# Kernel tuning notes

Measured on AMD Instinct MI355X. Metric: run time of the kernel, lower is better.

The kernel has to match this reference:

```python
import jax, jax.numpy as jnp
import numpy as np

D = 64      # d_model
H = 8       # n_head
HS = D // H # head_size = 8
EPS = 1e-5


def _layernorm(x, g, b):
    m = jnp.mean(x, axis=-1, keepdims=True)
    v = jnp.var(x, axis=-1, keepdims=True)
    return (x - m) * jax.lax.rsqrt(v + EPS) * g + b


def _attn(x, Wq, bq, Wk, bk, Wv, bv, Wp, bp, causal):
    # x: [B,T,D]; Wq/Wk/Wv: [H,D,HS]; bq/bk/bv: [H,HS]; Wp: [D,D]; bp: [D]
    B, T, _ = x.shape
    q = jnp.einsum('btd,hds->bhts', x, Wq) + bq[:, None, :]
    k = jnp.einsum('btd,hds->bhts', x, Wk) + bk[:, None, :]
    v = jnp.einsum('btd,hds->bhts', x, Wv) + bv[:, None, :]
    wei = jnp.einsum('bhts,bhus->bhtu', q, k) * (HS ** -0.5)
    if causal:
        mask = jnp.tril(jnp.ones((T, T), dtype=bool))
        wei = jnp.where(mask, wei, -jnp.inf)
    w = jax.nn.softmax(wei, axis=-1)
    out = jnp.einsum('bhtu,bhus->bhts', w, v)        # [B,H,T,HS]
    out = jnp.swapaxes(out, 1, 2).reshape(B, T, D)   # concat heads
    return out @ Wp + bp


def _ffn(x, W1, b1, W2, b2):
    return jax.nn.gelu(x @ W1 + b1, approximate=False) @ W2 + b2


def setup_inputs() -> dict:
    key = jax.random.key(0)
    ks = jax.random.split(key, 32)
    s = 0.02
    d = {'x': jax.random.normal(ks[0], (32768, 16, D), dtype=jnp.float32)}
    # unmasked attention params
    d['uWq'] = s * jax.random.normal(ks[1], (H, D, HS)); d['ubq'] = jnp.zeros((H, HS))
    d['uWk'] = s * jax.random.normal(ks[2], (H, D, HS)); d['ubk'] = jnp.zeros((H, HS))
    d['uWv'] = s * jax.random.normal(ks[3], (H, D, HS)); d['ubv'] = jnp.zeros((H, HS))
    d['uWp'] = s * jax.random.normal(ks[4], (D, D));     d['ubp'] = jnp.zeros((D,))
    # masked attention params
    d['mWq'] = s * jax.random.normal(ks[5], (H, D, HS)); d['mbq'] = jnp.zeros((H, HS))
    d['mWk'] = s * jax.random.normal(ks[6], (H, D, HS)); d['mbk'] = jnp.zeros((H, HS))
    d['mWv'] = s * jax.random.normal(ks[7], (H, D, HS)); d['mbv'] = jnp.zeros((H, HS))
    d['mWp'] = s * jax.random.normal(ks[8], (D, D));     d['mbp'] = jnp.zeros((D,))
    # feed-forward (shared across both FFN calls, as in the torch Block)
    d['fW1'] = s * jax.random.normal(ks[9], (D, 4 * D)); d['fb1'] = jnp.zeros((4 * D,))
    d['fW2'] = s * jax.random.normal(ks[10], (4 * D, D)); d['fb2'] = jnp.zeros((D,))
    # layernorms (norm1 and norm2 each reused twice, as in the torch Block)
    d['g1'] = jnp.ones((D,)); d['be1'] = jnp.zeros((D,))
    d['g2'] = jnp.ones((D,)); d['be2'] = jnp.zeros((D,))
    return d


def reference(x, uWq, ubq, uWk, ubk, uWv, ubv, uWp, ubp,
              mWq, mbq, mWk, mbk, mWv, mbv, mWp, mbp,
              fW1, fb1, fW2, fb2, g1, be1, g2, be2):
    x2 = x + _attn(_layernorm(x, g1, be1), uWq, ubq, uWk, ubk, uWv, ubv, uWp, ubp, causal=False)
    x = x2 + _ffn(_layernorm(x2, g2, be2), fW1, fb1, fW2, fb2)
    x2 = x + _attn(_layernorm(x, g1, be1), mWq, mbq, mWk, mbk, mWv, mbv, mWp, mbp, causal=True)
    x = x2 + _ffn(_layernorm(x2, g2, be2), fW1, fb1, fW2, fb2)
    return x
```

## Files before the change

kernel.cpp:

```cpp
#include <hip/hip_runtime.h>
#include <math.h>

typedef short bf16x8 __attribute__((ext_vector_type(8)));
typedef float f32x4 __attribute__((ext_vector_type(4)));

union BF { unsigned u[4]; bf16x8 v; };

__device__ __forceinline__ unsigned pk2(float a, float b) {
  unsigned ua = __float_as_uint(a), ub = __float_as_uint(b);
  ua = (ua + 0x7FFFu + ((ua >> 16) & 1u)) >> 16;
  ub = (ub + 0x7FFFu + ((ub >> 16) & 1u)) >> 16;
  return (ua & 0xFFFFu) | (ub << 16);
}

#define OFF_F1 32768
#define OFF_F2 49152

__global__ __launch_bounds__(256) void prep_w(
    const float* __restrict__ uWq, const float* __restrict__ uWk,
    const float* __restrict__ uWv, const float* __restrict__ uWp,
    const float* __restrict__ mWq, const float* __restrict__ mWk,
    const float* __restrict__ mWv, const float* __restrict__ mWp,
    const float* __restrict__ fW1, const float* __restrict__ fW2,
    unsigned short* __restrict__ ws)
{
  int e = blockIdx.x * blockDim.x + threadIdx.x;
  if (e >= 8192) return;
  int lane = e & 63;
  int fb   = e >> 6;
  int g = lane >> 4, li = lane & 15;
  unsigned short outv[8];
#pragma unroll
  for (int j = 0; j < 8; ++j) {
    float val;
    if (fb < 64) {
      int a  = fb >> 3;
      int mf = fb & 7;
      int m = mf >> 1, f = mf & 1;
      int k = f*32 + 4*g + (j&3) + 16*(j>>2);
      int n = 16*m + li;
      const float* W =
        (a==0)?uWq:(a==1)?uWk:(a==2)?uWv:(a==3)?uWp:
        (a==4)?mWq:(a==5)?mWk:(a==6)?mWv:mWp;
      if ((a & 3) != 3) val = W[(n>>3)*512 + k*8 + (n&7)];
      else              val = W[k*64 + n];
    } else if (fb < 96) {
      int mf = fb - 64;
      int m = mf >> 1, f = mf & 1;
      int k = f*32 + 4*g + (j&3) + 16*(j>>2);
      int n = 16*m + li;
      val = fW1[k*256 + n];
    } else {
      int mf = fb - 96;
      int m = mf >> 3, f = mf & 7;
      int k = f*32 + 4*g + (j&3) + 16*(j>>2);
      int n = 16*m + li;
      val = fW2[k*64 + n];
    }
    unsigned u = __float_as_uint(val);
    u = (u + 0x7FFFu + ((u >> 16) & 1u)) >> 16;
    outv[j] = (unsigned short)u;
  }
#pragma unroll
  for (int j = 0; j < 8; ++j) ws[(long)e*8 + j] = outv[j];
}

#define LDSP 72

__global__ __launch_bounds__(64, 2) void tblock_kern(
    const float* __restrict__ x,
    const float* __restrict__ ubq, const float* __restrict__ ubk,
    const float* __restrict__ ubv, const float* __restrict__ ubp,
    const float* __restrict__ mbq, const float* __restrict__ mbk,
    const float* __restrict__ mbv, const float* __restrict__ mbp,
    const float* __restrict__ fb1, const float* __restrict__ fb2,
    const float* __restrict__ g1, const float* __restrict__ be1,
    const float* __restrict__ g2, const float* __restrict__ be2,
    const unsigned short* __restrict__ wf,
    float* __restrict__ outp)
{
  __shared__ float KS[2][16][LDSP];
  __shared__ float VS[2][16][LDSP];

  const int lane = threadIdx.x;
  const int t = lane & 15, g = lane >> 4;
  const long sbase = (long)blockIdx.x * 2048;

  f32x4 R[2][4];
#pragma unroll
  for (int s = 0; s < 2; ++s)
#pragma unroll
    for (int m = 0; m < 4; ++m)
      R[s][m] = *(const f32x4*)(x + sbase + s*1024 + t*64 + 16*m + 4*g);

  auto ldA = [&](int base_bf16, int fbidx) -> bf16x8 {
    return *(const bf16x8*)(wf + base_bf16 + fbidx*512 + lane*8);
  };

  auto lnorm = [&](int s, const float* gp, const float* bp, BF bx[2]) {
    float sum = 0.f, sq = 0.f;
#pragma unroll
    for (int m = 0; m < 4; ++m)
#pragma unroll
      for (int r = 0; r < 4; ++r) { float v = R[s][m][r]; sum += v; sq += v*v; }
    sum += __shfl_xor(sum, 16); sum += __shfl_xor(sum, 32);
    sq  += __shfl_xor(sq , 16); sq  += __shfl_xor(sq , 32);
    float mean = sum * 0.015625f;
    float var  = sq  * 0.015625f - mean*mean;
    float rs = __builtin_amdgcn_rsqf(var + 1e-5f);
    float xn[4][4];
#pragma unroll
    for (int m = 0; m < 4; ++m) {
      f32x4 gm = *(const f32x4*)(gp + 16*m + 4*g);
      f32x4 bm = *(const f32x4*)(bp + 16*m + 4*g);
#pragma unroll
      for (int r = 0; r < 4; ++r)
        xn[m][r] = (R[s][m][r] - mean) * rs * gm[r] + bm[r];
    }
#pragma unroll
    for (int f = 0; f < 2; ++f)
#pragma unroll
      for (int mm = 0; mm < 2; ++mm) {
        bx[f].u[2*mm+0] = pk2(xn[2*f+mm][0], xn[2*f+mm][1]);
        bx[f].u[2*mm+1] = pk2(xn[2*f+mm][2], xn[2*f+mm][3]);
      }
  };

  auto attn = [&](int wq, int wk, int wv, int wp,
                  const float* bq, const float* bk, const float* bv,
                  const float* bpj, bool causal) {
    BF bx[2][2];
    lnorm(0, g1, be1, bx[0]);
    lnorm(1, g1, be1, bx[1]);

    f32x4 Q[2][4];
#pragma unroll
    for (int m = 0; m < 4; ++m) {
      bf16x8 a0 = ldA(wq, m*2+0), a1 = ldA(wq, m*2+1);
      f32x4 b4 = *(const f32x4*)(bq + 16*m + 4*g);
#pragma unroll
      for (int s = 0; s < 2; ++s) {
        f32x4 acc = {0.f,0.f,0.f,0.f};
        acc = __builtin_amdgcn_mfma_f32_16x16x32_bf16(a0, bx[s][0].v, acc, 0,0,0);
        acc = __builtin_amdgcn_mfma_f32_16x16x32_bf16(a1, bx[s][1].v, acc, 0,0,0);
#pragma unroll
        for (int r = 0; r < 4; ++r) acc[r] += b4[r];
        Q[s][m] = acc;
      }
    }
#pragma unroll
    for (int m = 0; m < 4; ++m) {
      bf16x8 a0 = ldA(wk, m*2+0), a1 = ldA(wk, m*2+1);
      f32x4 b4 = *(const f32x4*)(bk + 16*m + 4*g);
#pragma unroll
      for (int s = 0; s < 2; ++s) {
        f32x4 acc = {0.f,0.f,0.f,0.f};
        acc = __builtin_amdgcn_mfma_f32_16x16x32_bf16(a0, bx[s][0].v, acc, 0,0,0);
        acc = __builtin_amdgcn_mfma_f32_16x16x32_bf16(a1, bx[s][1].v, acc, 0,0,0);
#pragma unroll
        for (int r = 0; r < 4; ++r) acc[r] += b4[r];
        *(f32x4*)&KS[s][t][16*m + 4*g] = acc;
      }
    }
#pragma unroll
    for (int m = 0; m < 4; ++m) {
      bf16x8 a0 = ldA(wv, m*2+0), a1 = ldA(wv, m*2+1);
      f32x4 b4 = *(const f32x4*)(bv + 16*m + 4*g);
#pragma unroll
      for (int s = 0; s < 2; ++s) {
        f32x4 acc = {0.f,0.f,0.f,0.f};
        acc = __builtin_amdgcn_mfma_f32_16x16x32_bf16(a0, bx[s][0].v, acc, 0,0,0);
        acc = __builtin_amdgcn_mfma_f32_16x16x32_bf16(a1, bx[s][1].v, acc, 0,0,0);
#pragma unroll
        for (int r = 0; r < 4; ++r) acc[r] += b4[r];
        *(f32x4*)&VS[s][t][16*m + 4*g] = acc;
      }
    }

#pragma unroll
    for (int s = 0; s < 2; ++s) {
      f32x4 O[4];
#pragma unroll
      for (int mp = 0; mp < 2; ++mp) {
        float e[2][16];
#pragma unroll
        for (int u = 0; u < 16; ++u) {
          f32x4 k0 = *(const f32x4*)&KS[s][u][32*mp + 4*g];
          f32x4 k1 = *(const f32x4*)&KS[s][u][32*mp + 16 + 4*g];
          f32x4 q0 = Q[s][2*mp+0], q1 = Q[s][2*mp+1];
          e[0][u] = q0[0]*k0[0] + q0[1]*k0[1] + q0[2]*k0[2] + q0[3]*k0[3];
          e[1][u] = q1[0]*k1[0] + q1[1]*k1[1] + q1[2]*k1[2] + q1[3]*k1[3];
        }
#pragma unroll
        for (int mm = 0; mm < 2; ++mm)
#pragma unroll
          for (int u = 0; u < 16; ++u)
            e[mm][u] += __shfl_xor(e[mm][u], 16);
        float rden[2];
#pragma unroll
        for (int mm = 0; mm < 2; ++mm) {
          float den = 0.f;
#pragma unroll
          for (int u = 0; u < 16; ++u) {
            float ex = (causal && (u > t)) ? 0.f
                     : exp2f(e[mm][u] * 0.51006977f);
            e[mm][u] = ex; den += ex;
          }
          rden[mm] = __builtin_amdgcn_rcpf(den);
        }
        f32x4 acc0 = {0.f,0.f,0.f,0.f}, acc1 = {0.f,0.f,0.f,0.f};
#pragma unroll
        for (int u = 0; u < 16; ++u) {
          f32x4 v0 = *(const f32x4*)&VS[s][u][32*mp + 4*g];
          f32x4 v1 = *(const f32x4*)&VS[s][u][32*mp + 16 + 4*g];
#pragma unroll
          for (int r = 0; r < 4; ++r) {
            acc0[r] += e[0][u] * v0[r];
            acc1[r] += e[1][u] * v1[r];
          }
        }
#pragma unroll
        for (int r = 0; r < 4; ++r) {
          O[2*mp+0][r] = acc0[r] * rden[0];
          O[2*mp+1][r] = acc1[r] * rden[1];
        }
      }
#pragma unroll
      for (int f = 0; f < 2; ++f)
#pragma unroll
        for (int mm = 0; mm < 2; ++mm) {
          bx[s][f].u[2*mm+0] = pk2(O[2*f+mm][0], O[2*f+mm][1]);
          bx[s][f].u[2*mm+1] = pk2(O[2*f+mm][2], O[2*f+mm][3]);
        }
    }
#pragma unroll
    for (int m = 0; m < 4; ++m) {
      bf16x8 a0 = ldA(wp, m*2+0), a1 = ldA(wp, m*2+1);
      f32x4 b4 = *(const f32x4*)(bpj + 16*m + 4*g);
#pragma unroll
      for (int s = 0; s < 2; ++s) {
        f32x4 acc = {0.f,0.f,0.f,0.f};
        acc = __builtin_amdgcn_mfma_f32_16x16x32_bf16(a0, bx[s][0].v, acc, 0,0,0);
        acc = __builtin_amdgcn_mfma_f32_16x16x32_bf16(a1, bx[s][1].v, acc, 0,0,0);
#pragma unroll
        for (int r = 0; r < 4; ++r) R[s][m][r] += acc[r] + b4[r];
      }
    }
  };

  auto ffn = [&]() {
    BF bx[2][2];
    lnorm(0, g2, be2, bx[0]);
    lnorm(1, g2, be2, bx[1]);
    f32x4 yacc[2][4];
#pragma unroll
    for (int s = 0; s < 2; ++s)
#pragma unroll
      for (int m = 0; m < 4; ++m) yacc[s][m] = f32x4{0.f,0.f,0.f,0.f};
#pragma unroll
    for (int qt = 0; qt < 4; ++qt) {
      f32x4 h[2][4];
#pragma unroll
      for (int mt = 0; mt < 4; ++mt) {
        int ht = qt*4 + mt;
        bf16x8 a0 = ldA(OFF_F1, ht*2+0), a1 = ldA(OFF_F1, ht*2+1);
        f32x4 b4 = *(const f32x4*)(fb1 + 16*ht + 4*g);
#pragma unroll
        for (int s = 0; s < 2; ++s) {
          f32x4 acc = {0.f,0.f,0.f,0.f};
          acc = __builtin_amdgcn_mfma_f32_16x16x32_bf16(a0, bx[s][0].v, acc, 0,0,0);
          acc = __builtin_amdgcn_mfma_f32_16x16x32_bf16(a1, bx[s][1].v, acc, 0,0,0);
#pragma unroll
          for (int r = 0; r < 4; ++r) {
            float vv = acc[r] + b4[r];
            h[s][mt][r] = 0.5f * vv * (1.f + erff(vv * 0.70710678f));
          }
        }
      }
      BF bh[2][2];
#pragma unroll
      for (int s = 0; s < 2; ++s)
#pragma unroll
        for (int q2 = 0; q2 < 2; ++q2) {
          bh[s][q2].u[0] = pk2(h[s][2*q2+0][0], h[s][2*q2+0][1]);
          bh[s][q2].u[1] = pk2(h[s][2*q2+0][2], h[s][2*q2+0][3]);
          bh[s][q2].u[2] = pk2(h[s][2*q2+1][0], h[s][2*q2+1][1]);
          bh[s][q2].u[3] = pk2(h[s][2*q2+1][2], h[s][2*q2+1][3]);
        }
#pragma unroll
      for (int m = 0; m < 4; ++m)
#pragma unroll
        for (int q2 = 0; q2 < 2; ++q2) {
          bf16x8 a = ldA(OFF_F2, m*8 + qt*2 + q2);
#pragma unroll
          for (int s = 0; s < 2; ++s)
            yacc[s][m] = __builtin_amdgcn_mfma_f32_16x16x32_bf16(a, bh[s][q2].v, yacc[s][m], 0,0,0);
        }
    }
#pragma unroll
    for (int m = 0; m < 4; ++m) {
      f32x4 b4 = *(const f32x4*)(fb2 + 16*m + 4*g);
#pragma unroll
      for (int s = 0; s < 2; ++s)
#pragma unroll
        for (int r = 0; r < 4; ++r) R[s][m][r] += yacc[s][m][r] + b4[r];
    }
  };

  attn(0*4096, 1*4096, 2*4096, 3*4096, ubq, ubk, ubv, ubp, false);
  ffn();
  attn(4*4096, 5*4096, 6*4096, 7*4096, mbq, mbk, mbv, mbp, true);
  ffn();

#pragma unroll
  for (int s = 0; s < 2; ++s)
#pragma unroll
    for (int m = 0; m < 4; ++m)
      *(f32x4*)(outp + sbase + s*1024 + t*64 + 16*m + 4*g) = R[s][m];
}

extern "C" void kernel_launch(void* const* d_in, const int* in_sizes, int n_in,
                              void* d_out, int out_size, void* d_ws, size_t ws_size,
                              hipStream_t stream) {
  const float* x   = (const float*)d_in[0];
  const float* uWq = (const float*)d_in[1];
  const float* ubq = (const float*)d_in[2];
  const float* uWk = (const float*)d_in[3];
  const float* ubk = (const float*)d_in[4];
  const float* uWv = (const float*)d_in[5];
  const float* ubv = (const float*)d_in[6];
  const float* uWp = (const float*)d_in[7];
  const float* ubp = (const float*)d_in[8];
  const float* mWq = (const float*)d_in[9];
  const float* mbq = (const float*)d_in[10];
  const float* mWk = (const float*)d_in[11];
  const float* mbk = (const float*)d_in[12];
  const float* mWv = (const float*)d_in[13];
  const float* mbv = (const float*)d_in[14];
  const float* mWp = (const float*)d_in[15];
  const float* mbp = (const float*)d_in[16];
  const float* fW1 = (const float*)d_in[17];
  const float* fb1 = (const float*)d_in[18];
  const float* fW2 = (const float*)d_in[19];
  const float* fb2 = (const float*)d_in[20];
  const float* g1  = (const float*)d_in[21];
  const float* be1 = (const float*)d_in[22];
  const float* g2  = (const float*)d_in[23];
  const float* be2 = (const float*)d_in[24];

  unsigned short* ws = (unsigned short*)d_ws;

  prep_w<<<32, 256, 0, stream>>>(uWq, uWk, uWv, uWp, mWq, mWk, mWv, mWp,
                                 fW1, fW2, ws);
  tblock_kern<<<16384, 64, 0, stream>>>(x,
      ubq, ubk, ubv, ubp, mbq, mbk, mbv, mbp,
      fb1, fb2, g1, be1, g2, be2,
      (const unsigned short*)ws, (float*)d_out);
}
```

Measured before the change: 1.466 ms.

## Use tanh GELU, bf16 K/V in LDS, fused online softmax, bias-in-accumulator MFMAs

Replaces the erf-based GELU with a tanh-form approximation built from exp2 and a reciprocal. K and V are now stored as packed bf16 in shared memory instead of fp32, halving LDS traffic and footprint. The softmax and value accumulation are merged into a single loop over keys, so the per-row score arrays are gone. Biases are used as the initial MFMA accumulator, and the FFN output accumulates directly into the residual registers, which drops the separate yacc array. The tanh-form GELU and bf16 K/V both add numerical error compared with the reference.

Result: no change. 1.491 ms (+1.7%).

```diff
diff --git a/kernel.cpp b/kernel.cpp
--- a/kernel.cpp
+++ b/kernel.cpp
@@ -1,16 +1,27 @@
 #include <hip/hip_runtime.h>
-#include <math.h>
 
 typedef short bf16x8 __attribute__((ext_vector_type(8)));
 typedef float f32x4 __attribute__((ext_vector_type(4)));
-
-union BF { unsigned u[4]; bf16x8 v; };
+typedef unsigned u32x4 __attribute__((ext_vector_type(4)));
+typedef unsigned u32x2 __attribute__((ext_vector_type(2)));
 
 __device__ __forceinline__ unsigned pk2(float a, float b) {
   unsigned ua = __float_as_uint(a), ub = __float_as_uint(b);
   ua = (ua + 0x7FFFu + ((ua >> 16) & 1u)) >> 16;
   ub = (ub + 0x7FFFu + ((ub >> 16) & 1u)) >> 16;
   return (ua & 0xFFFFu) | (ub << 16);
+}
+__device__ __forceinline__ bf16x8 mkfrag(unsigned a, unsigned b, unsigned c, unsigned d) {
+  u32x4 t = {a, b, c, d};
+  return __builtin_bit_cast(bf16x8, t);
+}
+__device__ __forceinline__ float blo(unsigned u) { return __uint_as_float(u << 16); }
+__device__ __forceinline__ float bhi(unsigned u) { return __uint_as_float(u & 0xFFFF0000u); }
+
+__device__ __forceinline__ float gelu_f(float v) {
+  float y = 0.7978845608f * v * (1.f + 0.044715f * v * v);
+  float e = exp2f(y * 2.8853900818f);
+  return v * (1.f - __builtin_amdgcn_rcpf(e + 1.f));
 }
 
 #define OFF_F1 32768
@@ -65,7 +76,7 @@
   for (int j = 0; j < 8; ++j) ws[(long)e*8 + j] = outv[j];
 }
 
-#define LDSP 72
+#define NU 36
 
 __global__ __launch_bounds__(64, 2) void tblock_kern(
     const float* __restrict__ x,
@@ -79,8 +90,8 @@
     const unsigned short* __restrict__ wf,
     float* __restrict__ outp)
 {
-  __shared__ float KS[2][16][LDSP];
-  __shared__ float VS[2][16][LDSP];
+  __shared__ unsigned KS[2][16][NU];
+  __shared__ unsigned VS[2][16][NU];
 
   const int lane = threadIdx.x;
   const int t = lane & 15, g = lane >> 4;
@@ -97,7 +108,8 @@
     return *(const bf16x8*)(wf + base_bf16 + fbidx*512 + lane*8);
   };
 
-  auto lnorm = [&](int s, const float* gp, const float* bp, BF bx[2]) {
+  auto lnorm = [&](int s, const float* gp, const float* bp,
+                   bf16x8& b0, bf16x8& b1) {
     float sum = 0.f, sq = 0.f;
 #pragma unroll
     for (int m = 0; m < 4; ++m)
@@ -117,21 +129,18 @@
       for (int r = 0; r < 4; ++r)
         xn[m][r] = (R[s][m][r] - mean) * rs * gm[r] + bm[r];
     }
-#pragma unroll
-    for (int f = 0; f < 2; ++f)
-#pragma unroll
-      for (int mm = 0; mm < 2; ++mm) {
-        bx[f].u[2*mm+0] = pk2(xn[2*f+mm][0], xn[2*f+mm][1]);
-        bx[f].u[2*mm+1] = pk2(xn[2*f+mm][2], xn[2*f+mm][3]);
-      }
+    b0 = mkfrag(pk2(xn[0][0], xn[0][1]), pk2(xn[0][2], xn[0][3]),
+                pk2(xn[1][0], xn[1][1]), pk2(xn[1][2], xn[1][3]));
+    b1 = mkfrag(pk2(xn[2][0], xn[2][1]), pk2(xn[2][2], xn[2][3]),
+                pk2(xn[3][0], xn[3][1]), pk2(xn[3][2], xn[3][3]));
   };
 
   auto attn = [&](int wq, int wk, int wv, int wp,
                   const float* bq, const float* bk, const float* bv,
                   const float* bpj, bool causal) {
-    BF bx[2][2];
-    lnorm(0, g1, be1, bx[0]);
-    lnorm(1, g1, be1, bx[1]);
+    bf16x8 bx[2][2];
+    lnorm(0, g1, be1, bx[0][0], bx[0][1]);
+    lnorm(1, g1, be1, bx[1][0], bx[1][1]);
 
     f32x4 Q[2][4];
 #pragma unroll
@@ -139,14 +148,9 @@
       bf16x8 a0 = ldA(wq, m*2+0), a1 = ldA(wq, m*2+1);
       f32x4 b4 = *(const f32x4*)(bq + 16*m + 4*g);
 #pragma unroll
-      for (int s = 0; s < 2; ++s) {
-        f32x4 acc = {0.f,0.f,0.f,0.f};
-        acc = __builtin_amdgcn_mfma_f32_16x16x32_bf16(a0, bx[s][0].v, acc, 0,0,0);
-        acc = __builtin_amdgcn_mfma_f32_16x16x32_bf16(a1, bx[s][1].v, acc, 0,0,0);
-#pragma unroll
-        for (int r = 0; r < 4; ++r) acc[r] += b4[r];
-        Q[s][m] = acc;
-      }
+      for (int s = 0; s < 2; ++s)
+        Q[s][m] = __builtin_amdgcn_mfma_f32_16x16x32_bf16(
+            a1, bx[s][1], __builtin_amdgcn_mfma_f32_16x16x32_bf16(a0, bx[s][0], b4, 0,0,0), 0,0,0);
     }
 #pragma unroll
     for (int m = 0; m < 4; ++m) {
@@ -154,12 +158,9 @@
       f32x4 b4 = *(const f32x4*)(bk + 16*m + 4*g);
 #pragma unroll
       for (int s = 0; s < 2; ++s) {
-        f32x4 acc = {0.f,0.f,0.f,0.f};
-        acc = __builtin_amdgcn_mfma_f32_16x16x32_bf16(a0, bx[s][0].v, acc, 0,0,0);
-        acc = __builtin_amdgcn_mfma_f32_16x16x32_bf16(a1, bx[s][1].v, acc, 0,0,0);
-#pragma unroll
-        for (int r = 0; r < 4; ++r) acc[r] += b4[r];
-        *(f32x4*)&KS[s][t][16*m + 4*g] = acc;
+        f32x4 acc = __builtin_amdgcn_mfma_f32_16x16x32_bf16(
+            a1, bx[s][1], __builtin_amdgcn_mfma_f32_16x16x32_bf16(a0, bx[s][0], b4, 0,0,0), 0,0,0);
+        *(u32x2*)&KS[s][t][8*m + 2*g] = u32x2{pk2(acc[0], acc[1]), pk2(acc[2], acc[3])};
       }
     }
 #pragma unroll
@@ -168,12 +169,9 @@
       f32x4 b4 = *(const f32x4*)(bv + 16*m + 4*g);
 #pragma unroll
       for (int s = 0; s < 2; ++s) {
-        f32x4 acc = {0.f,0.f,0.f,0.f};
-        acc = __builtin_amdgcn_mfma_f32_16x16x32_bf16(a0, bx[s][0].v, acc, 0,0,0);
-        acc = __builtin_amdgcn_mfma_f32_16x16x32_bf16(a1, bx[s][1].v, acc, 0,0,0);
-#pragma unroll
-        for (int r = 0; r < 4; ++r) acc[r] += b4[r];
-        *(f32x4*)&VS[s][t][16*m + 4*g] = acc;
+        f32x4 acc = __builtin_amdgcn_mfma_f32_16x16x32_bf16(
+            a1, bx[s][1], __builtin_amdgcn_mfma_f32_16x16x32_bf16(a0, bx[s][0], b4, 0,0,0), 0,0,0);
+        *(u32x2*)&VS[s][t][8*m + 2*g] = u32x2{pk2(acc[0], acc[1]), pk2(acc[2], acc[3])};
       }
     }
 
@@ -182,128 +180,93 @@
       f32x4 O[4];
 #pragma unroll
       for (int mp = 0; mp < 2; ++mp) {
-        float e[2][16];
+        f32x4 q0 = Q[s][2*mp+0], q1 = Q[s][2*mp+1];
+        f32x4 acc0 = {0.f,0.f,0.f,0.f}, acc1 = {0.f,0.f,0.f,0.f};
+        float den0 = 0.f, den1 = 0.f;
 #pragma unroll
         for (int u = 0; u < 16; ++u) {
-          f32x4 k0 = *(const f32x4*)&KS[s][u][32*mp + 4*g];
-          f32x4 k1 = *(const f32x4*)&KS[s][u][32*mp + 16 + 4*g];
-          f32x4 q0 = Q[s][2*mp+0], q1 = Q[s][2*mp+1];
-          e[0][u] = q0[0]*k0[0] + q0[1]*k0[1] + q0[2]*k0[2] + q0[3]*k0[3];
-          e[1][u] = q1[0]*k1[0] + q1[1]*k1[1] + q1[2]*k1[2] + q1[3]*k1[3];
+          u32x2 kp0 = *(const u32x2*)&KS[s][u][16*mp + 2*g];
+          u32x2 kp1 = *(const u32x2*)&KS[s][u][16*mp + 8 + 2*g];
+          float d0 = q0[0]*blo(kp0[0]) + q0[1]*bhi(kp0[0])
+                   + q0[2]*blo(kp0[1]) + q0[3]*bhi(kp0[1]);
+          float d1 = q1[0]*blo(kp1[0]) + q1[1]*bhi(kp1[0])
+                   + q1[2]*blo(kp1[1]) + q1[3]*bhi(kp1[1]);
+          d0 += __shfl_xor(d0, 16);
+          d1 += __shfl_xor(d1, 16);
+          float ex0 = (causal && (u > t)) ? 0.f : exp2f(d0 * 0.51006977f);
+          float ex1 = (causal && (u > t)) ? 0.f : exp2f(d1 * 0.51006977f);
+          den0 += ex0; den1 += ex1;
+          u32x2 vp0 = *(const u32x2*)&VS[s][u][16*mp + 2*g];
+          u32x2 vp1 = *(const u32x2*)&VS[s][u][16*mp + 8 + 2*g];
+          acc0[0] += ex0*blo(vp0[0]); acc0[1] += ex0*bhi(vp0[0]);
+          acc0[2] += ex0*blo(vp0[1]); acc0[3] += ex0*bhi(vp0[1]);
+          acc1[0] += ex1*blo(vp1[0]); acc1[1] += ex1*bhi(vp1[0]);
+          acc1[2] += ex1*blo(vp1[1]); acc1[3] += ex1*bhi(vp1[1]);
         }
-#pragma unroll
-        for (int mm = 0; mm < 2; ++mm)
-#pragma unroll
-          for (int u = 0; u < 16; ++u)
-            e[mm][u] += __shfl_xor(e[mm][u], 16);
-        float rden[2];
-#pragma unroll
-        for (int mm = 0; mm < 2; ++mm) {
-          float den = 0.f;
-#pragma unroll
-          for (int u = 0; u < 16; ++u) {
-            float ex = (causal && (u > t)) ? 0.f
-                     : exp2f(e[mm][u] * 0.51006977f);
-            e[mm][u] = ex; den += ex;
-          }
-          rden[mm] = __builtin_amdgcn_rcpf(den);
-        }
-        f32x4 acc0 = {0.f,0.f,0.f,0.f}, acc1 = {0.f,0.f,0.f,0.f};
-#pragma unroll
-        for (int u = 0; u < 16; ++u) {
-          f32x4 v0 = *(const f32x4*)&VS[s][u][32*mp + 4*g];
-          f32x4 v1 = *(const f32x4*)&VS[s][u][32*mp + 16 + 4*g];
-#pragma unroll
-          for (int r = 0; r < 4; ++r) {
-            acc0[r] += e[0][u] * v0[r];
-            acc1[r] += e[1][u] * v1[r];
+        float rd0 = __builtin_amdgcn_rcpf(den0), rd1 = __builtin_amdgcn_rcpf(den1);
+#pragma unroll
+        for (int r = 0; r < 4; ++r) { O[2*mp+0][r] = acc0[r]*rd0; O[2*mp+1][r] = acc1[r]*rd1; }
+      }
+      bx[s][0] = mkfrag(pk2(O[0][0], O[0][1]), pk2(O[0][2], O[0][3]),
+                        pk2(O[1][0], O[1][1]), pk2(O[1][2], O[1][3]));
+      bx[s][1] = mkfrag(pk2(O[2][0], O[2][1]), pk2(O[2][2], O[2][3]),
+                        pk2(O[3][0], O[3][1]), pk2(O[3][2], O[3][3]));
+    }
+#pragma unroll
+    for (int m = 0; m < 4; ++m) {
+      bf16x8 a0 = ldA(wp, m*2+0), a1 = ldA(wp, m*2+1);
+      f32x4 b4 = *(const f32x4*)(bpj + 16*m + 4*g);
+#pragma unroll
+      for (int s = 0; s < 2; ++s) {
+        R[s][m] = __builtin_amdgcn_mfma_f32_16x16x32_bf16(
+            a1, bx[s][1], __builtin_amdgcn_mfma_f32_16x16x32_bf16(a0, bx[s][0], R[s][m], 0,0,0), 0,0,0);
+#pragma unroll
+        for (int r = 0; r < 4; ++r) R[s][m][r] += b4[r];
+      }
+    }
+  };
+
+  auto ffn = [&]() {
+    bf16x8 bx[2][2];
+    lnorm(0, g2, be2, bx[0][0], bx[0][1]);
+    lnorm(1, g2, be2, bx[1][0], bx[1][1]);
+#pragma unroll
+    for (int qt = 0; qt < 4; ++qt) {
+#pragma unroll
+      for (int q2 = 0; q2 < 2; ++q2) {
+        f32x4 h[2][2];
+#pragma unroll
+        for (int mt2 = 0; mt2 < 2; ++mt2) {
+          int ht = qt*4 + 2*q2 + mt2;
+          bf16x8 a0 = ldA(OFF_F1, ht*2+0), a1 = ldA(OFF_F1, ht*2+1);
+          f32x4 b4 = *(const f32x4*)(fb1 + 16*ht + 4*g);
+#pragma unroll
+          for (int s = 0; s < 2; ++s) {
+            f32x4 acc = __builtin_amdgcn_mfma_f32_16x16x32_bf16(
+                a1, bx[s][1], __builtin_amdgcn_mfma_f32_16x16x32_bf16(a0, bx[s][0], b4, 0,0,0), 0,0,0);
+#pragma unroll
+            for (int r = 0; r < 4; ++r) h[s][mt2][r] = gelu_f(acc[r]);
           }
         }
-#pragma unroll
-        for (int r = 0; r < 4; ++r) {
-          O[2*mp+0][r] = acc0[r] * rden[0];
-          O[2*mp+1][r] = acc1[r] * rden[1];
+        bf16x8 bh0 = mkfrag(pk2(h[0][0][0], h[0][0][1]), pk2(h[0][0][2], h[0][0][3]),
+                            pk2(h[0][1][0], h[0][1][1]), pk2(h[0][1][2], h[0][1][3]));
+        bf16x8 bh1 = mkfrag(pk2(h[1][0][0], h[1][0][1]), pk2(h[1][0][2], h[1][0][3]),
+                            pk2(h[1][1][0], h[1][1][1]), pk2(h[1][1][2], h[1][1][3]));
+#pragma unroll
+        for (int m = 0; m < 4; ++m) {
+          bf16x8 a = ldA(OFF_F2, m*8 + qt*2 + q2);
+          R[0][m] = __builtin_amdgcn_mfma_f32_16x16x32_bf16(a, bh0, R[0][m], 0,0,0);
+          R[1][m] = __builtin_amdgcn_mfma_f32_16x16x32_bf16(a, bh1, R[1][m], 0,0,0);
         }
       }
-#pragma unroll
-      for (int f = 0; f < 2; ++f)
-#pragma unroll
-        for (int mm = 0; mm < 2; ++mm) {
-          bx[s][f].u[2*mm+0] = pk2(O[2*f+mm][0], O[2*f+mm][1]);
-          bx[s][f].u[2*mm+1] = pk2(O[2*f+mm][2], O[2*f+mm][3]);
-        }
-    }
-#pragma unroll
-    for (int m = 0; m < 4; ++m) {
-      bf16x8 a0 = ldA(wp, m*2+0), a1 = ldA(wp, m*2+1);
-      f32x4 b4 = *(const f32x4*)(bpj + 16*m + 4*g);
-#pragma unroll
-      for (int s = 0; s < 2; ++s) {
-        f32x4 acc = {0.f,0.f,0.f,0.f};
-        acc = __builtin_amdgcn_mfma_f32_16x16x32_bf16(a0, bx[s][0].v, acc, 0,0,0);
-        acc = __builtin_amdgcn_mfma_f32_16x16x32_bf16(a1, bx[s][1].v, acc, 0,0,0);
-#pragma unroll
-        for (int r = 0; r < 4; ++r) R[s][m][r] += acc[r] + b4[r];
-      }
-    }
-  };
-
-  auto ffn = [&]() {
-    BF bx[2][2];
-    lnorm(0, g2, be2, bx[0]);
-    lnorm(1, g2, be2, bx[1]);
-    f32x4 yacc[2][4];
-#pragma unroll
-    for (int s = 0; s < 2; ++s)
-#pragma unroll
-      for (int m = 0; m < 4; ++m) yacc[s][m] = f32x4{0.f,0.f,0.f,0.f};
-#pragma unroll
-    for (int qt = 0; qt < 4; ++qt) {
-      f32x4 h[2][4];
-#pragma unroll
-      for (int mt = 0; mt < 4; ++mt) {
-        int ht = qt*4 + mt;
-        bf16x8 a0 = ldA(OFF_F1, ht*2+0), a1 = ldA(OFF_F1, ht*2+1);
-        f32x4 b4 = *(const f32x4*)(fb1 + 16*ht + 4*g);
-#pragma unroll
-        for (int s = 0; s < 2; ++s) {
-          f32x4 acc = {0.f,0.f,0.f,0.f};
-          acc = __builtin_amdgcn_mfma_f32_16x16x32_bf16(a0, bx[s][0].v, acc, 0,0,0);
-          acc = __builtin_amdgcn_mfma_f32_16x16x32_bf16(a1, bx[s][1].v, acc, 0,0,0);
-#pragma unroll
-          for (int r = 0; r < 4; ++r) {
-            float vv = acc[r] + b4[r];
-            h[s][mt][r] = 0.5f * vv * (1.f + erff(vv * 0.70710678f));
-          }
-        }
-      }
-      BF bh[2][2];
+    }
+#pragma unroll
+    for (int m = 0; m < 4; ++m) {
+      f32x4 b4 = *(const f32x4*)(fb2 + 16*m + 4*g);
 #pragma unroll
       for (int s = 0; s < 2; ++s)
 #pragma unroll
-        for (int q2 = 0; q2 < 2; ++q2) {
-          bh[s][q2].u[0] = pk2(h[s][2*q2+0][0], h[s][2*q2+0][1]);
-          bh[s][q2].u[1] = pk2(h[s][2*q2+0][2], h[s][2*q2+0][3]);
-          bh[s][q2].u[2] = pk2(h[s][2*q2+1][0], h[s][2*q2+1][1]);
-          bh[s][q2].u[3] = pk2(h[s][2*q2+1][2], h[s][2*q2+1][3]);
-        }
-#pragma unroll
-      for (int m = 0; m < 4; ++m)
-#pragma unroll
-        for (int q2 = 0; q2 < 2; ++q2) {
-          bf16x8 a = ldA(OFF_F2, m*8 + qt*2 + q2);
-#pragma unroll
-          for (int s = 0; s < 2; ++s)
-            yacc[s][m] = __builtin_amdgcn_mfma_f32_16x16x32_bf16(a, bh[s][q2].v, yacc[s][m], 0,0,0);
-        }
-    }
-#pragma unroll
-    for (int m = 0; m < 4; ++m) {
-      f32x4 b4 = *(const f32x4*)(fb2 + 16*m + 4*g);
-#pragma unroll
-      for (int s = 0; s < 2; ++s)
-#pragma unroll
-        for (int r = 0; r < 4; ++r) R[s][m][r] += yacc[s][m][r] + b4[r];
+        for (int r = 0; r < 4; ++r) R[s][m][r] += b4[r];
     }
   };
 
```
